# Kernel optimization log

Measured on AMD Instinct MI355X. Metric: run time of the kernel, lower is better.

## Reference

```python
import math
import jax, jax.numpy as jnp
import numpy as np

B = 256          # graphs per batch
N0 = 512         # nodes per graph
DEG = 16         # avg degree
E = B * N0 * DEG # total edges
F_IN = 160
H = 64
RATIO = 0.11
NUM_CLASSES = 2


def setup_inputs() -> dict:
    key = jax.random.key(0)
    ks = jax.random.split(key, 20)
    x = jax.random.normal(ks[0], (B * N0, F_IN), jnp.float32)
    # within-graph random edges: src/dst local in [0, N0) plus graph offset
    eg = E // B
    off = (jnp.arange(B, dtype=jnp.int32) * N0)[:, None]
    src = (jax.random.randint(ks[1], (B, eg), 0, N0, jnp.int32) + off).reshape(-1)
    dst = (jax.random.randint(ks[2], (B, eg), 0, N0, jnp.int32) + off).reshape(-1)
    edge_index = jnp.stack([src, dst], 0)
    s = lambda fan: 1.0 / np.sqrt(fan)
    inp = {
        'x': x,
        'edge_index': edge_index,
        'conv1_Wr': jax.random.normal(ks[3], (F_IN, H), jnp.float32) * s(F_IN),
        'conv1_Wl': jax.random.normal(ks[4], (F_IN, H), jnp.float32) * s(F_IN),
        'conv1_b': jnp.zeros((H,), jnp.float32),
        'convs_Wr': jax.random.normal(ks[5], (5, H, H), jnp.float32) * s(H),
        'convs_Wl': jax.random.normal(ks[6], (5, H, H), jnp.float32) * s(H),
        'convs_b': jnp.zeros((5, H), jnp.float32),
        'pools_Wr': jax.random.normal(ks[7], (2, H, 1), jnp.float32) * s(H),
        'pools_Wl': jax.random.normal(ks[8], (2, H, 1), jnp.float32) * s(H),
        'pools_b': jnp.zeros((2, 1), jnp.float32),
        'lin1_W': jax.random.normal(ks[9], (6 * H, H), jnp.float32) * s(6 * H),
        'lin1_b': jnp.zeros((H,), jnp.float32),
        'lin2_W': jax.random.normal(ks[10], (H, NUM_CLASSES), jnp.float32) * s(H),
        'lin2_b': jnp.zeros((NUM_CLASSES,), jnp.float32),
    }
    return inp


def _gconv(x, src, dst, emask, Wr, Wl, b, n_nodes):
    # PyG GraphConv(aggr='mean'): lin_rel(mean_{j->i} x_j) + lin_root(x)
    msg = x[src] * emask[:, None]                              # [E, F]
    agg = jax.ops.segment_sum(msg, dst, num_segments=n_nodes)  # [N, F]
    deg = jax.ops.segment_sum(emask, dst, num_segments=n_nodes)
    agg = agg / jnp.maximum(deg, 1.0)[:, None]
    return agg @ Wr + b + x @ Wl


def _sag_pool(x, src, dst, emask, Wr, Wl, b, n_per, k):
    n_nodes = B * n_per
    score = _gconv(x, src, dst, emask, Wr, Wl, b, n_nodes)[:, 0]   # [N]
    _, idx = jax.lax.top_k(score.reshape(B, n_per), k)             # [B, k]
    perm = (idx + (jnp.arange(B, dtype=jnp.int32) * n_per)[:, None]).reshape(-1)
    new_x = x[perm] * jnp.tanh(score[perm])[:, None]
    newpos = jnp.full((n_nodes,), -1, jnp.int32).at[perm].set(
        jnp.arange(B * k, dtype=jnp.int32))
    ns, nd = newpos[src], newpos[dst]
    valid = (ns >= 0) & (nd >= 0)
    new_emask = emask * valid.astype(emask.dtype)
    return new_x, jnp.where(valid, ns, 0), jnp.where(valid, nd, 0), new_emask


def _gmp(x, n_per):  # global_mean_pool with equal-size graphs
    return x.reshape(B, n_per, -1).mean(axis=1)


def reference(x, edge_index, conv1_Wr, conv1_Wl, conv1_b, convs_Wr, convs_Wl,
              convs_b, pools_Wr, pools_Wl, pools_b, lin1_W, lin1_b,
              lin2_W, lin2_b):
    src, dst = edge_index[0], edge_index[1]
    emask = jnp.ones(src.shape, x.dtype)
    n = N0
    x = jax.nn.relu(_gconv(x, src, dst, emask, conv1_Wr, conv1_Wl, conv1_b, B * n))
    xs = [_gmp(x, n)]
    for i in range(5):
        x = jax.nn.relu(_gconv(x, src, dst, emask, convs_Wr[i], convs_Wl[i],
                               convs_b[i], B * n))
        xs.append(_gmp(x, n))
        if i % 2 == 0 and i < 4:
            j = i // 2
            k = math.ceil(RATIO * n)
            x, src, dst, emask = _sag_pool(x, src, dst, emask, pools_Wr[j],
                                           pools_Wl[j], pools_b[j], n, k)
            n = k
    h = jnp.concatenate(xs, axis=-1)          # JumpingKnowledge('cat') -> [B, 6H]
    h = jax.nn.relu(h @ lin1_W + lin1_b)
    h = h @ lin2_W + lin2_b                   # dropout is identity in eval mode
    return jax.nn.log_softmax(h, axis=-1)
```

## Files before the change

kernel.cpp:

```cpp
#include <hip/hip_runtime.h>
#include <math.h>

namespace {
constexpr int NB   = 256;
constexpr int EPG  = 8192;
constexpr int ETOT = NB * EPG;
constexpr int FH   = 64;
constexpr int NN0  = NB * 512;
}

__device__ float g_feat[3][(size_t)NN0 * FH];
__device__ float g_xs[NB * 6 * FH];
__device__ int   g_esrc[2][ETOT];
__device__ int   g_edst[2][ETOT];
__device__ int   g_ecnt[2][NB];
__device__ unsigned short g_csr[ETOT];
__device__ unsigned int   g_deg[NN0], g_start[NN0];

template<int K>
__global__ __launch_bounds__(256)
void mm_dual(const float* __restrict__ xext, int in_idx,
             const float* __restrict__ Wr, const float* __restrict__ Wl,
             const float* __restrict__ bias, int zr_idx, int xl_idx)
{
  constexpr int RPB = 64;
  constexpr int KC  = 32;
  __shared__ float xs[RPB][KC];
  __shared__ float wrT[KC/4][64][4];
  __shared__ float wlT[KC/4][64][4];
  const float* __restrict__ x = (in_idx < 0) ? xext : g_feat[in_idx];
  float* __restrict__ zr = g_feat[zr_idx];
  float* __restrict__ xl = g_feat[xl_idx];
  const int t = threadIdx.x;
  const int rowbase = blockIdx.x * RPB;
  const int f  = t & 31;
  const int rg = t >> 5;
  const int wv = t >> 6;
  const int wc = t & 63;
  const int wq = t >> 6;
  float ar0[8], ar1[8], al0[8], al1[8];
  #pragma unroll
  for (int r = 0; r < 8; ++r) { ar0[r]=0.f; ar1[r]=0.f; al0[r]=0.f; al1[r]=0.f; }

  for (int c = 0; c < K / KC; ++c) {
    __syncthreads();
    #pragma unroll
    for (int i = 0; i < 2; ++i) {
      const int idx = t + i * 256;
      const int r = idx >> 3, q = idx & 7;
      const float* gp = &x[(size_t)(rowbase + r) * K + c * KC + q * 4];
      float* lp = &xs[0][0] + (size_t)(i * 256 + wv * 64) * 4;
      __builtin_amdgcn_global_load_lds(
          (const __attribute__((address_space(1))) unsigned int*)gp,
          (__attribute__((address_space(3))) unsigned int*)lp, 16, 0, 0);
    }
    #pragma unroll
    for (int h = 0; h < 2; ++h) {
      const int kq = wq * 2 + h;
      #pragma unroll
      for (int i = 0; i < 4; ++i) {
        const int krow = c * KC + kq * 4 + i;
        wrT[kq][wc][i] = Wr[(size_t)krow * 64 + wc];
        wlT[kq][wc][i] = Wl[(size_t)krow * 64 + wc];
      }
    }
    __syncthreads();
    #pragma unroll 1
    for (int k4 = 0; k4 < KC / 4; ++k4) {
      const float4 wr0 = *reinterpret_cast<const float4*>(&wrT[k4][f][0]);
      const float4 wr1 = *reinterpret_cast<const float4*>(&wrT[k4][f+32][0]);
      const float4 wl0 = *reinterpret_cast<const float4*>(&wlT[k4][f][0]);
      const float4 wl1 = *reinterpret_cast<const float4*>(&wlT[k4][f+32][0]);
      #pragma unroll
      for (int r = 0; r < 8; ++r) {
        const float4 xv = *reinterpret_cast<const float4*>(&xs[rg*8 + r][k4*4]);
        float a0 = ar0[r], a1 = ar1[r], b0 = al0[r], b1 = al1[r];
        a0 = fmaf(xv.x, wr0.x, a0); a0 = fmaf(xv.y, wr0.y, a0);
        a0 = fmaf(xv.z, wr0.z, a0); a0 = fmaf(xv.w, wr0.w, a0);
        a1 = fmaf(xv.x, wr1.x, a1); a1 = fmaf(xv.y, wr1.y, a1);
        a1 = fmaf(xv.z, wr1.z, a1); a1 = fmaf(xv.w, wr1.w, a1);
        b0 = fmaf(xv.x, wl0.x, b0); b0 = fmaf(xv.y, wl0.y, b0);
        b0 = fmaf(xv.z, wl0.z, b0); b0 = fmaf(xv.w, wl0.w, b0);
        b1 = fmaf(xv.x, wl1.x, b1); b1 = fmaf(xv.y, wl1.y, b1);
        b1 = fmaf(xv.z, wl1.z, b1); b1 = fmaf(xv.w, wl1.w, b1);
        ar0[r] = a0; ar1[r] = a1; al0[r] = b0; al1[r] = b1;
      }
    }
  }
  const float bv0 = bias[f], bv1 = bias[f + 32];
  #pragma unroll
  for (int r = 0; r < 8; ++r) {
    const size_t row = (size_t)(rowbase + rg * 8 + r);
    zr[row * 64 + f]      = ar0[r];
    zr[row * 64 + f + 32] = ar1[r];
    xl[row * 64 + f]      = al0[r] + bv0;
    xl[row * 64 + f + 32] = al1[r] + bv1;
  }
}

__global__ __launch_bounds__(1024)
void agg_full_build(int zr_idx, int xl_idx,
                    const int* __restrict__ esrc, const int* __restrict__ edst,
                    int out_idx, int xs_off)
{
  __shared__ float zlds[512 * 64];
  __shared__ unsigned short csr[EPG];
  __shared__ unsigned int hist[512], bufA[512], bufB[512];
  __shared__ float red[16][64];
  const float* __restrict__ zr  = g_feat[zr_idx];
  const float* __restrict__ xlb = g_feat[xl_idx];
  float* __restrict__ xout = g_feat[out_idx];
  const int g = blockIdx.x, t = threadIdx.x;
  const int gbase = g * 512, ebase = g * EPG;
  if (t < 512) hist[t] = 0;
  __syncthreads();
  {
    const float4* zsrc = reinterpret_cast<const float4*>(zr + (size_t)gbase * 64);
    float4* zdst = reinterpret_cast<float4*>(zlds);
    #pragma unroll
    for (int i = 0; i < 8; ++i) zdst[t + i * 1024] = zsrc[t + i * 1024];
  }
  for (int e = t; e < EPG; e += 1024)
    atomicAdd(&hist[edst[ebase + e] - gbase], 1u);
  __syncthreads();
  if (t < 512) bufA[t] = hist[t];
  __syncthreads();
  unsigned int *pa = bufA, *pb = bufB;
  for (int off = 1; off < 512; off <<= 1) {
    if (t < 512) {
      unsigned int v = pa[t];
      if (t >= off) v += pa[t - off];
      pb[t] = v;
    }
    __syncthreads();
    unsigned int* tmp = pa; pa = pb; pb = tmp;
  }
  unsigned int excl = 0;
  if (t < 512) excl = pa[t] - hist[t];
  __syncthreads();
  if (t < 512) { bufA[t] = excl; bufB[t] = excl; }
  __syncthreads();
  for (int e = t; e < EPG; e += 1024) {
    const int sl = esrc[ebase + e] - gbase;
    const int dl = edst[ebase + e] - gbase;
    const unsigned int pos = atomicAdd(&bufB[dl], 1u);
    csr[pos] = (unsigned short)sl;
  }
  __syncthreads();
  if (t < 512) { g_deg[gbase + t] = hist[t]; g_start[gbase + t] = bufA[t]; }
  {
    unsigned int* gcsr32 = reinterpret_cast<unsigned int*>(&g_csr[ebase]);
    const unsigned int* lcsr32 = reinterpret_cast<const unsigned int*>(csr);
    for (int i = t; i < EPG/2; i += 1024) gcsr32[i] = lcsr32[i];
  }
  const int lane = t & 63, w = t >> 6;
  float psum = 0.f;
  for (int nd = w; nd < 512; nd += 16) {
    const unsigned int s = bufA[nd], d = hist[nd];
    float a0 = 0.f, a1 = 0.f, a2 = 0.f, a3 = 0.f;
    unsigned int j = 0;
    for (; j + 4 <= d; j += 4) {
      const int i0 = csr[s+j], i1 = csr[s+j+1], i2 = csr[s+j+2], i3 = csr[s+j+3];
      a0 += zlds[i0*64 + lane]; a1 += zlds[i1*64 + lane];
      a2 += zlds[i2*64 + lane]; a3 += zlds[i3*64 + lane];
    }
    for (; j < d; ++j) a0 += zlds[csr[s+j]*64 + lane];
    const float acc = (a0 + a1) + (a2 + a3);
    float v = acc / (float)(d > 0 ? d : 1) + xlb[(size_t)(gbase + nd)*64 + lane];
    v = fmaxf(v, 0.f);
    xout[(size_t)(gbase + nd)*64 + lane] = v;
    psum += v;
  }
  red[w][lane] = psum;
  __syncthreads();
  if (t < 64) {
    float s = 0.f;
    #pragma unroll
    for (int ww = 0; ww < 16; ++ww) s += red[ww][t];
    g_xs[g*384 + xs_off + t] = s * (1.f/512.f);
  }
}

__global__ __launch_bounds__(1024)
void conv_agg_fused(int x_idx, const float* __restrict__ Wr,
                    const float* __restrict__ Wl, const float* __restrict__ bias,
                    int out_idx, int xs_off)
{
  __shared__ float zlds[512 * 64];
  __shared__ unsigned short csr[EPG];
  __shared__ unsigned int hist[512], start[512];
  __shared__ float w_r[1024], w_l[1024];
  const float* __restrict__ X1 = g_feat[x_idx];
  float* __restrict__ xout = g_feat[out_idx];
  const int g = blockIdx.x, t = threadIdx.x;
  const int gbase = g * 512, ebase = g * EPG;
  const int lane = t & 63, w = t >> 6;
  {
    const float4* src = reinterpret_cast<const float4*>(X1 + (size_t)gbase * 64);
    float4* dst = reinterpret_cast<float4*>(zlds);
    #pragma unroll
    for (int i = 0; i < 8; ++i) dst[t + i * 1024] = src[t + i * 1024];
  }
  if (t < 512) { hist[t] = g_deg[gbase + t]; start[t] = g_start[gbase + t]; }
  {
    const uint4* c4 = reinterpret_cast<const uint4*>(&g_csr[ebase]);
    uint4* l4 = reinterpret_cast<uint4*>(csr);
    l4[t] = c4[t];
  }
  const int ndbase = w * 32;
  float zacc[32], xla[32];
  #pragma unroll
  for (int i = 0; i < 32; ++i) { zacc[i] = 0.f; xla[i] = 0.f; }
  #pragma unroll 1
  for (int c = 0; c < 4; ++c) {
    __syncthreads();
    w_r[t] = Wr[c * 1024 + t];
    w_l[t] = Wl[c * 1024 + t];
    __syncthreads();
    #pragma unroll 1
    for (int k4 = 0; k4 < 4; ++k4) {
      const int kb = k4 * 4;
      const float wr0 = w_r[(kb+0)*64 + lane], wr1 = w_r[(kb+1)*64 + lane],
                  wr2 = w_r[(kb+2)*64 + lane], wr3 = w_r[(kb+3)*64 + lane];
      const float wl0 = w_l[(kb+0)*64 + lane], wl1 = w_l[(kb+1)*64 + lane],
                  wl2 = w_l[(kb+2)*64 + lane], wl3 = w_l[(kb+3)*64 + lane];
      #pragma unroll
      for (int i = 0; i < 32; ++i) {
        const float4 xv = *reinterpret_cast<const float4*>(
            &zlds[(ndbase + i) * 64 + c * 16 + kb]);
        float za = zacc[i], xa = xla[i];
        za = fmaf(xv.x, wr0, za); za = fmaf(xv.y, wr1, za);
        za = fmaf(xv.z, wr2, za); za = fmaf(xv.w, wr3, za);
        xa = fmaf(xv.x, wl0, xa); xa = fmaf(xv.y, wl1, xa);
        xa = fmaf(xv.z, wl2, xa); xa = fmaf(xv.w, wl3, xa);
        zacc[i] = za; xla[i] = xa;
      }
    }
  }
  __syncthreads();
  #pragma unroll
  for (int i = 0; i < 32; ++i)
    zlds[(ndbase + i) * 64 + lane] = zacc[i];
  __syncthreads();
  const float bv = bias[lane];
  float psum = 0.f;
  #pragma unroll 1
  for (int i = 0; i < 32; ++i) {
    const int nd = ndbase + i;
    const unsigned int s = start[nd], d = hist[nd];
    float a0 = 0.f, a1 = 0.f, a2 = 0.f, a3 = 0.f;
    unsigned int j = 0;
    for (; j + 4 <= d; j += 4) {
      const int i0 = csr[s+j], i1 = csr[s+j+1], i2 = csr[s+j+2], i3 = csr[s+j+3];
      a0 += zlds[i0*64 + lane]; a1 += zlds[i1*64 + lane];
      a2 += zlds[i2*64 + lane]; a3 += zlds[i3*64 + lane];
    }
    for (; j < d; ++j) a0 += zlds[csr[s+j]*64 + lane];
    float v = ((a0 + a1) + (a2 + a3)) / (float)(d > 0 ? d : 1) + xla[i] + bv;
    v = fmaxf(v, 0.f);
    xout[(size_t)(gbase + nd)*64 + lane] = v;
    psum += v;
  }
  __syncthreads();
  zlds[w * 64 + lane] = psum;
  __syncthreads();
  if (t < 64) {
    float s = 0.f;
    #pragma unroll
    for (int ww = 0; ww < 16; ++ww) s += zlds[ww*64 + t];
    g_xs[g*384 + xs_off + t] = s * (1.f/512.f);
  }
}

__global__ __launch_bounds__(512)
void sag_pool0(int in_idx,
               const int* __restrict__ esrc, const int* __restrict__ edst,
               const float* __restrict__ wr, const float* __restrict__ wl,
               const float* __restrict__ pb,
               int xnew_idx, int out_stage)
{
  constexpr int NPER = 512, NPOW2 = 512, KSEL = 57;
  __shared__ float zs[NPER], swl[NPER], sscore[NPER];
  __shared__ unsigned long long keys[NPOW2];
  __shared__ unsigned short pcsr[EPG];
  __shared__ short newpos[NPER];
  __shared__ int scnt;
  const float* __restrict__ xin = g_feat[in_idx];
  float* __restrict__ xnew = g_feat[xnew_idx];
  int* __restrict__ eosrc = g_esrc[out_stage];
  int* __restrict__ eodst = g_edst[out_stage];
  const int g = blockIdx.x, t = threadIdx.x;
  const int gbase = g * NPER, ebase = g * EPG;
  const int lane = t & 63, w = t >> 6;
  const float wrv = wr[lane], wlv = wl[lane];
  for (int nd = w; nd < NPER; nd += 8) {
    const float v = xin[(size_t)(gbase + nd)*64 + lane];
    float a = v * wrv, b = v * wlv;
    #pragma unroll
    for (int off = 32; off > 0; off >>= 1) {
      a += __shfl_xor(a, off);
      b += __shfl_xor(b, off);
    }
    if (lane == 0) { zs[nd] = a; swl[nd] = b; }
  }
  {
    const unsigned int* gcsr32 = reinterpret_cast<const unsigned int*>(&g_csr[ebase]);
    unsigned int* lcsr32 = reinterpret_cast<unsigned int*>(pcsr);
    for (int i = t; i < EPG/2; i += 512) lcsr32[i] = gcsr32[i];
  }
  if (t == 0) scnt = 0;
  __syncthreads();
  if (t < NPER) {
    const unsigned int s = g_start[gbase + t], d = g_deg[gbase + t];
    float a = 0.f;
    for (unsigned int j = 0; j < d; ++j) a += zs[pcsr[s + j]];
    sscore[t] = a / fmaxf((float)d, 1.f) + pb[0] + swl[t];
  }
  __syncthreads();
  if (t < NPOW2) {
    unsigned long long key = 0ull;
    if (t < NPER) {
      unsigned int u = __float_as_uint(sscore[t]);
      u = (u & 0x80000000u) ? ~u : (u | 0x80000000u);
      key = ((unsigned long long)u << 32) | (unsigned int)(~(unsigned int)t);
    }
    keys[t] = key;
  }
  __syncthreads();
  for (int kk = 2; kk <= NPOW2; kk <<= 1) {
    for (int j = kk >> 1; j > 0; j >>= 1) {
      if (t < NPOW2) {
        const int ixj = t ^ j;
        if (ixj > t) {
          const unsigned long long a = keys[t], bk = keys[ixj];
          const bool up = ((t & kk) == 0);
          if (up ? (a < bk) : (a > bk)) { keys[t] = bk; keys[ixj] = a; }
        }
      }
      __syncthreads();
    }
  }
  if (t < NPER) newpos[t] = -1;
  __syncthreads();
  if (t < KSEL)
    newpos[(int)(~(unsigned int)(keys[t] & 0xffffffffull))] = (short)t;
  __syncthreads();
  for (int r = w; r < KSEL; r += 8) {
    const int old = (int)(~(unsigned int)(keys[r] & 0xffffffffull));
    const float sc = tanhf(sscore[old]);
    xnew[(size_t)(g*KSEL + r)*64 + lane] =
        xin[(size_t)(gbase + old)*64 + lane] * sc;
  }
  for (int e = t; e < EPG; e += 512) {
    const int sl = esrc[ebase + e] - gbase;
    const int dl = edst[ebase + e] - gbase;
    const int ns = newpos[sl], nd2 = newpos[dl];
    if (ns >= 0 && nd2 >= 0) {
      const int slot = atomicAdd(&scnt, 1);
      eosrc[ebase + slot] = g*KSEL + ns;
      eodst[ebase + slot] = g*KSEL + nd2;
    }
  }
  __syncthreads();
  if (t == 0) g_ecnt[out_stage][g] = scnt;
}

__device__ __forceinline__ void conv_small(
    float* X, float* Z, float* ACC, float* w_s, const float* deg,
    const float* Wr, const float* Wl, const float* bias,
    int n, const int* esrc, const int* edst, int m, int gb, int ebase,
    int xs_off, int g, int t, int lane, int w)
{
  for (int i = t; i < n*64; i += 512) { Z[i] = 0.f; ACC[i] = 0.f; }
  __syncthreads();
  for (int kc = 0; kc < 4; ++kc) {
    for (int i = t; i < 1024; i += 512) w_s[i] = Wr[kc*1024 + i];
    __syncthreads();
    for (int r = w; r < n; r += 8) {
      float zacc = 0.f;
      #pragma unroll
      for (int k = 0; k < 16; ++k)
        zacc = fmaf(X[r*64 + kc*16 + k], w_s[k*64 + lane], zacc);
      Z[r*64 + lane] += zacc;
    }
    __syncthreads();
  }
  for (int e = w; e < m; e += 8) {
    const int sl = esrc[ebase + e] - gb;
    const int dl = edst[ebase + e] - gb;
    atomicAdd(&ACC[dl*64 + lane], Z[sl*64 + lane]);
  }
  __syncthreads();
  for (int i = t; i < n*64; i += 512) {
    const int r = i >> 6, f = i & 63;
    Z[i] = ACC[i] / fmaxf(deg[r], 1.f) + bias[f];
  }
  __syncthreads();
  for (int kc = 0; kc < 4; ++kc) {
    for (int i = t; i < 1024; i += 512) w_s[i] = Wl[kc*1024 + i];
    __syncthreads();
    for (int r = w; r < n; r += 8) {
      float zacc = 0.f;
      #pragma unroll
      for (int k = 0; k < 16; ++k)
        zacc = fmaf(X[r*64 + kc*16 + k], w_s[k*64 + lane], zacc);
      Z[r*64 + lane] += zacc;
    }
    __syncthreads();
  }
  for (int i = t; i < n*64; i += 512) X[i] = fmaxf(Z[i], 0.f);
  __syncthreads();
  if (t < 64) {
    float s = 0.f;
    for (int r = 0; r < n; ++r) s += X[r*64 + t];
    g_xs[g*384 + xs_off + t] = s / (float)n;
  }
  __syncthreads();
}

__global__ __launch_bounds__(512)
void tail(const float* __restrict__ cWr, const float* __restrict__ cWl,
          const float* __restrict__ cb,
          const float* __restrict__ pWr, const float* __restrict__ pWl,
          const float* __restrict__ pb)
{
  __shared__ float X[57*64], Z[57*64], ACC[57*64];
  __shared__ float w_s[16*64];
  __shared__ float deg[64];
  __shared__ float zs[64], swl[64], sagg[64], sscore[64];
  __shared__ unsigned long long keys[64];
  __shared__ short newpos[64];
  __shared__ int scnt;
  const int g = blockIdx.x, t = threadIdx.x;
  const int lane = t & 63, w = t >> 6;
  const int ebase = g * EPG;

  for (int i = t; i < 57*64; i += 512) X[i] = g_feat[0][(size_t)(g*57)*64 + i];
  const int m0 = g_ecnt[0][g];
  if (t < 64) deg[t] = 0.f;
  __syncthreads();
  for (int e = t; e < m0; e += 512)
    atomicAdd(&deg[g_edst[0][ebase + e] - g*57], 1.f);
  __syncthreads();

  conv_small(X, Z, ACC, w_s, deg, cWr + 4096,  cWl + 4096,  cb + 64,
             57, g_esrc[0], g_edst[0], m0, g*57, ebase, 128, g, t, lane, w);
  conv_small(X, Z, ACC, w_s, deg, cWr + 8192,  cWl + 8192,  cb + 128,
             57, g_esrc[0], g_edst[0], m0, g*57, ebase, 192, g, t, lane, w);

  {
    const float pwrv = pWr[64 + lane], pwlv = pWl[64 + lane];
    for (int r = w; r < 57; r += 8) {
      float a = X[r*64 + lane] * pwrv, b = X[r*64 + lane] * pwlv;
      #pragma unroll
      for (int off = 32; off > 0; off >>= 1) {
        a += __shfl_xor(a, off);
        b += __shfl_xor(b, off);
      }
      if (lane == 0) { zs[r] = a; swl[r] = b; }
    }
    if (t < 64) sagg[t] = 0.f;
    if (t == 0) scnt = 0;
    __syncthreads();
    for (int e = t; e < m0; e += 512)
      atomicAdd(&sagg[g_edst[0][ebase + e] - g*57],
                zs[g_esrc[0][ebase + e] - g*57]);
    __syncthreads();
    if (t < 57) sscore[t] = sagg[t] / fmaxf(deg[t], 1.f) + pb[1] + swl[t];
    __syncthreads();
    if (t < 64) {
      unsigned long long key = 0ull;
      if (t < 57) {
        unsigned int u = __float_as_uint(sscore[t]);
        u = (u & 0x80000000u) ? ~u : (u | 0x80000000u);
        key = ((unsigned long long)u << 32) | (unsigned int)(~(unsigned int)t);
      }
      keys[t] = key;
    }
    __syncthreads();
    for (int kk = 2; kk <= 64; kk <<= 1) {
      for (int j = kk >> 1; j > 0; j >>= 1) {
        if (t < 64) {
          const int ixj = t ^ j;
          if (ixj > t) {
            const unsigned long long a = keys[t], bk = keys[ixj];
            const bool up = ((t & kk) == 0);
            if (up ? (a < bk) : (a > bk)) { keys[t] = bk; keys[ixj] = a; }
          }
        }
        __syncthreads();
      }
    }
    if (t < 64) newpos[t] = -1;
    __syncthreads();
    if (t < 7)
      newpos[(int)(~(unsigned int)(keys[t] & 0xffffffffull))] = (short)t;
    __syncthreads();
    for (int r = w; r < 7; r += 8) {
      const int old = (int)(~(unsigned int)(keys[r] & 0xffffffffull));
      const float sc = tanhf(sscore[old]);
      Z[r*64 + lane] = X[old*64 + lane] * sc;
    }
    for (int e = t; e < m0; e += 512) {
      const int sl = g_esrc[0][ebase + e] - g*57;
      const int dl = g_edst[0][ebase + e] - g*57;
      const int ns = newpos[sl], nd2 = newpos[dl];
      if (ns >= 0 && nd2 >= 0) {
        const int slot = atomicAdd(&scnt, 1);
        g_esrc[1][ebase + slot] = g*7 + ns;
        g_edst[1][ebase + slot] = g*7 + nd2;
      }
    }
    __syncthreads();
    for (int i = t; i < 7*64; i += 512) X[i] = Z[i];
    if (t < 64) deg[t] = 0.f;
    __syncthreads();
  }
  const int m1 = scnt;
  for (int e = t; e < m1; e += 512)
    atomicAdd(&deg[g_edst[1][ebase + e] - g*7], 1.f);
  __syncthreads();

  conv_small(X, Z, ACC, w_s, deg, cWr + 12288, cWl + 12288, cb + 192,
             7, g_esrc[1], g_edst[1], m1, g*7, ebase, 256, g, t, lane, w);
  conv_small(X, Z, ACC, w_s, deg, cWr + 16384, cWl + 16384, cb + 256,
             7, g_esrc[1], g_edst[1], m1, g*7, ebase, 320, g, t, lane, w);
}

__global__ __launch_bounds__(64)
void head(const float* __restrict__ W1, const float* __restrict__ b1,
          const float* __restrict__ W2, const float* __restrict__ b2,
          float* __restrict__ out)
{
  __shared__ float h[384], o1[64], lg[2];
  const int g = blockIdx.x, t = threadIdx.x;
  for (int i = t; i < 384; i += 64) h[i] = g_xs[g*384 + i];
  __syncthreads();
  float acc = b1[t];
  for (int j = 0; j < 384; ++j) acc = fmaf(h[j], W1[j*64 + t], acc);
  o1[t] = fmaxf(acc, 0.f);
  __syncthreads();
  if (t < 2) {
    float a2 = b2[t];
    for (int f2 = 0; f2 < 64; ++f2) a2 = fmaf(o1[f2], W2[f2*2 + t], a2);
    lg[t] = a2;
  }
  __syncthreads();
  if (t < 2) {
    const float mx = fmaxf(lg[0], lg[1]);
    const float lse = mx + logf(expf(lg[0]-mx) + expf(lg[1]-mx));
    out[g*2 + t] = lg[t] - lse;
  }
}

extern "C" void kernel_launch(void* const* d_in, const int* in_sizes, int n_in,
                              void* d_out, int out_size, void* d_ws, size_t ws_size,
                              hipStream_t stream)
{
  (void)in_sizes; (void)n_in; (void)d_ws; (void)ws_size; (void)out_size;
  const float* x    = (const float*)d_in[0];
  const int*   ei   = (const int*)d_in[1];
  const float* c1Wr = (const float*)d_in[2];
  const float* c1Wl = (const float*)d_in[3];
  const float* c1b  = (const float*)d_in[4];
  const float* cWr  = (const float*)d_in[5];
  const float* cWl  = (const float*)d_in[6];
  const float* cb   = (const float*)d_in[7];
  const float* pWr  = (const float*)d_in[8];
  const float* pWl  = (const float*)d_in[9];
  const float* pb   = (const float*)d_in[10];
  const float* l1W  = (const float*)d_in[11];
  const float* l1b  = (const float*)d_in[12];
  const float* l2W  = (const float*)d_in[13];
  const float* l2b  = (const float*)d_in[14];
  float* out = (float*)d_out;
  const int* esrc = ei;
  const int* edst = ei + ETOT;

  mm_dual<160><<<NN0/64, 256, 0, stream>>>(x, -1, c1Wr, c1Wl, c1b, 0, 1);
  agg_full_build<<<NB, 1024, 0, stream>>>(0, 1, esrc, edst, 1, 0);
  conv_agg_fused<<<NB, 1024, 0, stream>>>(1, cWr, cWl, cb, 2, 64);
  sag_pool0<<<NB, 512, 0, stream>>>(2, esrc, edst, pWr, pWl, pb, 0, 0);
  tail<<<NB, 512, 0, stream>>>(cWr, cWl, cb, pWr, pWl, pb);
  head<<<NB, 64, 0, stream>>>(l1W, l1b, l2W, l2b, out);
}
```

Measured before the change: 365.6 us.

## Fuse second conv layer with first SAG pooling into one per-graph kernel

Merges conv_agg_fused and sag_pool0 into a single 1024-thread kernel per graph. The conv output stays in LDS and feeds the pooling score, sort and selection directly, so the full [N,64] intermediate is never written to or reread from global memory. The CSR and degree arrays are reused from LDS, and one launch is removed. Shared buffers are aliased (weights, keys, newpos) to fit LDS, which adds syncs and makes the pooling phase run at 1024-thread occupancy.

New measurement: 341.2 us. 6.7% less time.

```diff
diff --git a/kernel.cpp b/kernel.cpp
--- a/kernel.cpp
+++ b/kernel.cpp
@@ -182,19 +182,26 @@
 }
 
 __global__ __launch_bounds__(1024)
-void conv_agg_fused(int x_idx, const float* __restrict__ Wr,
-                    const float* __restrict__ Wl, const float* __restrict__ bias,
-                    int out_idx, int xs_off)
+void conv_agg_pool(int x_idx, const float* __restrict__ Wr,
+                   const float* __restrict__ Wl, const float* __restrict__ bias,
+                   const int* __restrict__ esrc, const int* __restrict__ edst,
+                   const float* __restrict__ pwr, const float* __restrict__ pwl,
+                   const float* __restrict__ pb,
+                   int xnew_idx, int xs_off)
 {
   __shared__ float zlds[512 * 64];
-  __shared__ unsigned short csr[EPG];
-  __shared__ unsigned int hist[512], start[512];
-  __shared__ float w_r[1024], w_l[1024];
+  __shared__ unsigned short csrbuf[EPG];
+  __shared__ __align__(16) unsigned long long u2[512];
+  __shared__ float wpf[2048];
+  __shared__ int scnt;
+  unsigned int* hist  = reinterpret_cast<unsigned int*>(u2);
+  unsigned int* start = hist + 512;
   const float* __restrict__ X1 = g_feat[x_idx];
-  float* __restrict__ xout = g_feat[out_idx];
+  float* __restrict__ xnew = g_feat[xnew_idx];
   const int g = blockIdx.x, t = threadIdx.x;
   const int gbase = g * 512, ebase = g * EPG;
   const int lane = t & 63, w = t >> 6;
+  const int ndbase = w * 32;
   {
     const float4* src = reinterpret_cast<const float4*>(X1 + (size_t)gbase * 64);
     float4* dst = reinterpret_cast<float4*>(zlds);
@@ -204,13 +211,15 @@
   if (t < 512) { hist[t] = g_deg[gbase + t]; start[t] = g_start[gbase + t]; }
   {
     const uint4* c4 = reinterpret_cast<const uint4*>(&g_csr[ebase]);
-    uint4* l4 = reinterpret_cast<uint4*>(csr);
+    uint4* l4 = reinterpret_cast<uint4*>(csrbuf);
     l4[t] = c4[t];
   }
-  const int ndbase = w * 32;
+  if (t == 0) scnt = 0;
   float zacc[32], xla[32];
   #pragma unroll
   for (int i = 0; i < 32; ++i) { zacc[i] = 0.f; xla[i] = 0.f; }
+  float* w_r = wpf;
+  float* w_l = wpf + 1024;
   #pragma unroll 1
   for (int c = 0; c < 4; ++c) {
     __syncthreads();
@@ -251,51 +260,37 @@
     float a0 = 0.f, a1 = 0.f, a2 = 0.f, a3 = 0.f;
     unsigned int j = 0;
     for (; j + 4 <= d; j += 4) {
-      const int i0 = csr[s+j], i1 = csr[s+j+1], i2 = csr[s+j+2], i3 = csr[s+j+3];
+      const int i0 = csrbuf[s+j], i1 = csrbuf[s+j+1],
+                i2 = csrbuf[s+j+2], i3 = csrbuf[s+j+3];
       a0 += zlds[i0*64 + lane]; a1 += zlds[i1*64 + lane];
       a2 += zlds[i2*64 + lane]; a3 += zlds[i3*64 + lane];
     }
-    for (; j < d; ++j) a0 += zlds[csr[s+j]*64 + lane];
+    for (; j < d; ++j) a0 += zlds[csrbuf[s+j]*64 + lane];
     float v = ((a0 + a1) + (a2 + a3)) / (float)(d > 0 ? d : 1) + xla[i] + bv;
     v = fmaxf(v, 0.f);
-    xout[(size_t)(gbase + nd)*64 + lane] = v;
+    zacc[i] = v;
     psum += v;
   }
   __syncthreads();
-  zlds[w * 64 + lane] = psum;
+  #pragma unroll
+  for (int i = 0; i < 32; ++i)
+    zlds[(ndbase + i) * 64 + lane] = zacc[i];
+  wpf[w * 64 + lane] = psum;
   __syncthreads();
   if (t < 64) {
     float s = 0.f;
     #pragma unroll
-    for (int ww = 0; ww < 16; ++ww) s += zlds[ww*64 + t];
+    for (int ww = 0; ww < 16; ++ww) s += wpf[ww*64 + t];
     g_xs[g*384 + xs_off + t] = s * (1.f/512.f);
   }
-}
-
-__global__ __launch_bounds__(512)
-void sag_pool0(int in_idx,
-               const int* __restrict__ esrc, const int* __restrict__ edst,
-               const float* __restrict__ wr, const float* __restrict__ wl,
-               const float* __restrict__ pb,
-               int xnew_idx, int out_stage)
-{
-  constexpr int NPER = 512, NPOW2 = 512, KSEL = 57;
-  __shared__ float zs[NPER], swl[NPER], sscore[NPER];
-  __shared__ unsigned long long keys[NPOW2];
-  __shared__ unsigned short pcsr[EPG];
-  __shared__ short newpos[NPER];
-  __shared__ int scnt;
-  const float* __restrict__ xin = g_feat[in_idx];
-  float* __restrict__ xnew = g_feat[xnew_idx];
-  int* __restrict__ eosrc = g_esrc[out_stage];
-  int* __restrict__ eodst = g_edst[out_stage];
-  const int g = blockIdx.x, t = threadIdx.x;
-  const int gbase = g * NPER, ebase = g * EPG;
-  const int lane = t & 63, w = t >> 6;
-  const float wrv = wr[lane], wlv = wl[lane];
-  for (int nd = w; nd < NPER; nd += 8) {
-    const float v = xin[(size_t)(gbase + nd)*64 + lane];
-    float a = v * wrv, b = v * wlv;
+  __syncthreads();
+  float* zs     = wpf;
+  float* swl    = wpf + 512;
+  float* sscore = wpf + 1024;
+  const float pwrv = pwr[lane], pwlv = pwl[lane];
+  for (int nd = w; nd < 512; nd += 16) {
+    const float v = zlds[nd*64 + lane];
+    float a = v * pwrv, b = v * pwlv;
     #pragma unroll
     for (int off = 32; off > 0; off >>= 1) {
       a += __shfl_xor(a, off);
@@ -303,33 +298,24 @@
     }
     if (lane == 0) { zs[nd] = a; swl[nd] = b; }
   }
-  {
-    const unsigned int* gcsr32 = reinterpret_cast<const unsigned int*>(&g_csr[ebase]);
-    unsigned int* lcsr32 = reinterpret_cast<unsigned int*>(pcsr);
-    for (int i = t; i < EPG/2; i += 512) lcsr32[i] = gcsr32[i];
-  }
-  if (t == 0) scnt = 0;
-  __syncthreads();
-  if (t < NPER) {
-    const unsigned int s = g_start[gbase + t], d = g_deg[gbase + t];
+  __syncthreads();
+  if (t < 512) {
+    const unsigned int s = start[t], d = hist[t];
     float a = 0.f;
-    for (unsigned int j = 0; j < d; ++j) a += zs[pcsr[s + j]];
+    for (unsigned int j = 0; j < d; ++j) a += zs[csrbuf[s + j]];
     sscore[t] = a / fmaxf((float)d, 1.f) + pb[0] + swl[t];
   }
   __syncthreads();
-  if (t < NPOW2) {
-    unsigned long long key = 0ull;
-    if (t < NPER) {
-      unsigned int u = __float_as_uint(sscore[t]);
-      u = (u & 0x80000000u) ? ~u : (u | 0x80000000u);
-      key = ((unsigned long long)u << 32) | (unsigned int)(~(unsigned int)t);
-    }
-    keys[t] = key;
-  }
-  __syncthreads();
-  for (int kk = 2; kk <= NPOW2; kk <<= 1) {
+  unsigned long long* keys = u2;
+  if (t < 512) {
+    unsigned int u = __float_as_uint(sscore[t]);
+    u = (u & 0x80000000u) ? ~u : (u | 0x80000000u);
+    keys[t] = ((unsigned long long)u << 32) | (unsigned int)(~(unsigned int)t);
+  }
+  __syncthreads();
+  for (int kk = 2; kk <= 512; kk <<= 1) {
     for (int j = kk >> 1; j > 0; j >>= 1) {
-      if (t < NPOW2) {
+      if (t < 512) {
         const int ixj = t ^ j;
         if (ixj > t) {
           const unsigned long long a = keys[t], bk = keys[ixj];
@@ -340,29 +326,29 @@
       __syncthreads();
     }
   }
-  if (t < NPER) newpos[t] = -1;
-  __syncthreads();
-  if (t < KSEL)
-    newpos[(int)(~(unsigned int)(keys[t] & 0xffffffffull))] = (short)t;
-  __syncthreads();
-  for (int r = w; r < KSEL; r += 8) {
+  short* np = reinterpret_cast<short*>(csrbuf);
+  if (t < 512) np[t] = -1;
+  __syncthreads();
+  if (t < 57)
+    np[(int)(~(unsigned int)(keys[t] & 0xffffffffull))] = (short)t;
+  __syncthreads();
+  for (int r = w; r < 57; r += 16) {
     const int old = (int)(~(unsigned int)(keys[r] & 0xffffffffull));
     const float sc = tanhf(sscore[old]);
-    xnew[(size_t)(g*KSEL + r)*64 + lane] =
-        xin[(size_t)(gbase + old)*64 + lane] * sc;
-  }
-  for (int e = t; e < EPG; e += 512) {
+    xnew[(size_t)(g*57 + r)*64 + lane] = zlds[old*64 + lane] * sc;
+  }
+  for (int e = t; e < EPG; e += 1024) {
     const int sl = esrc[ebase + e] - gbase;
     const int dl = edst[ebase + e] - gbase;
-    const int ns = newpos[sl], nd2 = newpos[dl];
+    const int ns = np[sl], nd2 = np[dl];
     if (ns >= 0 && nd2 >= 0) {
       const int slot = atomicAdd(&scnt, 1);
-      eosrc[ebase + slot] = g*KSEL + ns;
-      eodst[ebase + slot] = g*KSEL + nd2;
-    }
-  }
-  __syncthreads();
-  if (t == 0) g_ecnt[out_stage][g] = scnt;
+      g_esrc[0][ebase + slot] = g*57 + ns;
+      g_edst[0][ebase + slot] = g*57 + nd2;
+    }
+  }
+  __syncthreads();
+  if (t == 0) g_ecnt[0][g] = scnt;
 }
 
 __device__ __forceinline__ void conv_small(
@@ -579,8 +565,8 @@
 
   mm_dual<160><<<NN0/64, 256, 0, stream>>>(x, -1, c1Wr, c1Wl, c1b, 0, 1);
   agg_full_build<<<NB, 1024, 0, stream>>>(0, 1, esrc, edst, 1, 0);
-  conv_agg_fused<<<NB, 1024, 0, stream>>>(1, cWr, cWl, cb, 2, 64);
-  sag_pool0<<<NB, 512, 0, stream>>>(2, esrc, edst, pWr, pWl, pb, 0, 0);
+  conv_agg_pool<<<NB, 1024, 0, stream>>>(1, cWr, cWl, cb, esrc, edst,
+                                         pWr, pWl, pb, 0, 64);
   tail<<<NB, 512, 0, stream>>>(cWr, cWl, cb, pWr, pWl, pb);
   head<<<NB, 64, 0, stream>>>(l1W, l1b, l2W, l2b, out);
 }
```
